# Optimization experiments

Hardware: AMD Instinct MI355X
Metric: run time of the kernel (lower is better)

Reference implementation:

```python
import jax, jax.numpy as jnp
import numpy as np

E, H, M = 1024, 16, 256
B, S = 2, 2048
D = E // H
SCALE = D ** -0.5


def setup_inputs() -> dict:
    key = jax.random.key(0)
    ks = jax.random.split(key, 10)
    p = 0.02
    return {
        "x": jax.random.normal(ks[0], (B, S, E), jnp.float32),
        "Wq": jax.random.normal(ks[1], (E, E), jnp.float32) * p,
        "bq": jax.random.normal(ks[2], (E,), jnp.float32) * p,
        "Wk": jax.random.normal(ks[3], (E, E), jnp.float32) * p,
        "bk": jax.random.normal(ks[4], (E,), jnp.float32) * p,
        "Wv": jax.random.normal(ks[5], (E, E), jnp.float32) * p,
        "bv": jax.random.normal(ks[6], (E,), jnp.float32) * p,
        "Wo": jax.random.normal(ks[7], (E, E), jnp.float32) * p,
        "bo": jax.random.normal(ks[8], (E,), jnp.float32) * p,
        "memory_state": jax.random.normal(ks[9], (M, E), jnp.float32) * p,
    }


def reference(x, Wq, bq, Wk, bk, Wv, bv, Wo, bo, memory_state):
    b, s, e = x.shape
    # QKV projections (torch Linear: y = x W^T + b), split heads -> [b,h,s,d]
    q = (x @ Wq.T + bq).reshape(b, s, H, D).transpose(0, 2, 1, 3)
    k = (x @ Wk.T + bk).reshape(b, s, H, D).transpose(0, 2, 1, 3)
    v = (x @ Wv.T + bv).reshape(b, s, H, D).transpose(0, 2, 1, 3)
    # full self-attention (eval mode: dropout is identity)
    attn = jax.nn.softmax(jnp.einsum("bhqd,bhkd->bhqk", q, k) * SCALE, axis=-1)
    attn_out = jnp.einsum("bhqk,bhkd->bhqd", attn, v)
    attn_out = attn_out.transpose(0, 2, 1, 3).reshape(b, s, e)
    # memory-read cross-attention on raw x against compressed memory [M,E]
    mem_w = jax.nn.softmax(jnp.einsum("bse,me->bsm", x, memory_state) * SCALE, axis=-1)
    mem_out = jnp.einsum("bsm,me->bse", mem_w, memory_state)
    out = attn_out + 0.5 * mem_out
    return out @ Wo.T + bo
```

## Files before the change

kernel.cpp:

```cpp
#include <hip/hip_runtime.h>
#include <cstdint>
#include <cstddef>


typedef __bf16 bf16;
typedef bf16  bf16x8 __attribute__((ext_vector_type(8)));
typedef bf16  bf16x4 __attribute__((ext_vector_type(4)));
typedef float f32x4  __attribute__((ext_vector_type(4)));
typedef int   i32x4  __attribute__((ext_vector_type(4)));

#define B_DIM 2
#define S_DIM 2048
#define E_DIM 1024
#define H_DIM 16
#define D_DIM 64
#define M_DIM 256
#define NROW  (B_DIM * S_DIM)
#define C1 0.18033688011112042f

__device__ __forceinline__ void async_cp16(const bf16* g, bf16* l)
{
    __builtin_amdgcn_global_load_lds(
        (const __attribute__((address_space(1))) void*)g,
        (__attribute__((address_space(3))) void*)l, 16, 0, 0);
}

__global__ void __launch_bounds__(256)
conv_all(const float* __restrict__ x,  const float* __restrict__ Wq,
         const float* __restrict__ Wk, const float* __restrict__ Wv,
         const float* __restrict__ Wo, const float* __restrict__ mem,
         bf16* __restrict__ xb,  bf16* __restrict__ Wqb,
         bf16* __restrict__ Wkb, bf16* __restrict__ Wvb,
         bf16* __restrict__ Wob, bf16* __restrict__ memb,
         bf16* __restrict__ memt)
{
    int t = blockIdx.x * 256 + threadIdx.x;
    const float* src; bf16* dst; int off; bool is_mem = false;
    if      (t <  524288) { src = x;   dst = xb;   off = t; }
    else if (t <  655360) { src = Wq;  dst = Wqb;  off = t - 524288; }
    else if (t <  786432) { src = Wk;  dst = Wkb;  off = t - 655360; }
    else if (t <  917504) { src = Wv;  dst = Wvb;  off = t - 786432; }
    else if (t < 1048576) { src = Wo;  dst = Wob;  off = t - 917504; }
    else                  { src = mem; dst = memb; off = t - 1048576; is_mem = true; }
    const float4* p = (const float4*)src + (size_t)off * 2;
    float4 a = p[0], b = p[1];
    bf16x8 o;
    o[0] = (bf16)a.x; o[1] = (bf16)a.y; o[2] = (bf16)a.z; o[3] = (bf16)a.w;
    o[4] = (bf16)b.x; o[5] = (bf16)b.y; o[6] = (bf16)b.z; o[7] = (bf16)b.w;
    *(bf16x8*)(dst + (size_t)off * 8) = o;
    if (is_mem) {
        int r = off >> 7, c0 = (off & 127) * 8;
        float h[8] = {a.x, a.y, a.z, a.w, b.x, b.y, b.z, b.w};
#pragma unroll
        for (int j = 0; j < 8; ++j)
            memt[(size_t)(c0 + j) * M_DIM + r] = (bf16)(0.5f * h[j]);
    }
}

struct GemmAcc { f32x4 a[4][4]; };

__device__ __forceinline__ void
gemm_core(const bf16* __restrict__ A, const bf16* __restrict__ Bm,
          int K, int m0, int n0, bf16* As, bf16* Bs, GemmAcc& R)
{
    const int tid  = threadIdx.x;
    const int lane = tid & 63;
    const int wave = tid >> 6;
    const int quad = lane >> 4;
    const int l16  = lane & 15;
    const int wm   = (wave >> 1) * 64;
    const int wn   = (wave & 1) * 64;

#pragma unroll
    for (int i = 0; i < 4; ++i)
#pragma unroll
        for (int j = 0; j < 4; ++j)
            R.a[i][j] = f32x4{0.f, 0.f, 0.f, 0.f};

    int s_c0  = wave * 128 + lane;
    int s_r0  = s_c0 >> 2;
    int s_k0  = (s_c0 & 3) ^ ((s_r0 >> 1) & 3);
    int s_c1  = s_c0 + 64;
    int s_r1  = s_c1 >> 2;
    int s_k1  = (s_c1 & 3) ^ ((s_r1 >> 1) & 3);
    const bf16* gA0 = A  + (size_t)(m0 + s_r0) * K + s_k0 * 8;
    const bf16* gA1 = A  + (size_t)(m0 + s_r1) * K + s_k1 * 8;
    const bf16* gB0 = Bm + (size_t)(n0 + s_r0) * K + s_k0 * 8;
    const bf16* gB1 = Bm + (size_t)(n0 + s_r1) * K + s_k1 * 8;

#define STAGE(buf, k0)                                                     \
    do {                                                                   \
        async_cp16(gA0 + (k0), &As[(buf) * 4096 + wave * 1024]);           \
        async_cp16(gA1 + (k0), &As[(buf) * 4096 + wave * 1024 + 512]);     \
        async_cp16(gB0 + (k0), &Bs[(buf) * 4096 + wave * 1024]);           \
        async_cp16(gB1 + (k0), &Bs[(buf) * 4096 + wave * 1024 + 512]);     \
    } while (0)

    STAGE(0, 0);
    int buf = 0;
    for (int k0 = 0; k0 < K; k0 += 32) {
        __syncthreads();
        if (k0 + 32 < K) STAGE(buf ^ 1, k0 + 32);

        const bf16* Ab = As + buf * 4096;
        const bf16* Bb = Bs + buf * 4096;
        bf16x8 af[4], bfr[4];
#pragma unroll
        for (int mi = 0; mi < 4; ++mi) {
            int m    = wm + mi * 16 + l16;
            int slot = quad ^ ((m >> 1) & 3);
            af[mi]   = *(const bf16x8*)(&Ab[(m * 4 + slot) * 8]);
        }
#pragma unroll
        for (int ni = 0; ni < 4; ++ni) {
            int n    = wn + ni * 16 + l16;
            int slot = quad ^ ((n >> 1) & 3);
            bfr[ni]  = *(const bf16x8*)(&Bb[(n * 4 + slot) * 8]);
        }
#pragma unroll
        for (int mi = 0; mi < 4; ++mi)
#pragma unroll
            for (int ni = 0; ni < 4; ++ni)
                R.a[mi][ni] = __builtin_amdgcn_mfma_f32_16x16x32_bf16(
                    af[mi], bfr[ni], R.a[mi][ni], 0, 0, 0);
        buf ^= 1;
    }
#undef STAGE
}

__global__ void __launch_bounds__(256, 3)
gemm_qkvl(const bf16* __restrict__ A,
          const bf16* __restrict__ Wq, const bf16* __restrict__ Wk,
          const bf16* __restrict__ Wv, const bf16* __restrict__ memb,
          const float* __restrict__ bq, const float* __restrict__ bk,
          const float* __restrict__ bv,
          bf16* __restrict__ q, bf16* __restrict__ k,
          bf16* __restrict__ vt, bf16* __restrict__ lg)
{
    __shared__ __align__(16) bf16 As[2 * 4096];
    __shared__ __align__(16) bf16 Bs[2 * 4096];
    const int lid  = blockIdx.x;
    const int xcd  = lid & 7;
    const int idx  = lid >> 3;
    const int mloc = idx / 26;
    const int nn   = idx - mloc * 26;
    const int m0   = (mloc * 8 + xcd) * 128;
    const int widx = (nn < 24) ? (nn >> 3) : 3;
    const int n0   = (nn < 24) ? (nn & 7) * 128 : (nn - 24) * 128;
    const bf16*  Bm = (widx == 0) ? Wq : (widx == 1) ? Wk :
                      (widx == 2) ? Wv : memb;
    GemmAcc R;
    gemm_core(A, Bm, E_DIM, m0, n0, As, Bs, R);

    const int lane = threadIdx.x & 63, wave = threadIdx.x >> 6;
    const int quad = lane >> 4, l16 = lane & 15;
    const int wm = (wave >> 1) * 64, wn = (wave & 1) * 64;

    if (widx == 0 || widx == 1) {
        bf16* C = (widx == 0) ? q : k;
        const float* bi = (widx == 0) ? bq : bk;
        float scale = (widx == 0) ? C1 : 1.0f;
#pragma unroll
        for (int ni = 0; ni < 4; ++ni) {
            int col  = n0 + wn + ni * 16 + l16;
            float bb = bi[col];
#pragma unroll
            for (int mi = 0; mi < 4; ++mi)
#pragma unroll
                for (int r = 0; r < 4; ++r) {
                    int rowg = m0 + wm + mi * 16 + quad * 4 + r;
                    C[(size_t)rowg * E_DIM + col] =
                        (bf16)((R.a[mi][ni][r] + bb) * scale);
                }
        }
    } else if (widx == 2) {
#pragma unroll
        for (int ni = 0; ni < 4; ++ni) {
            int col = n0 + wn + ni * 16 + l16;
            float bb = bv[col];
#pragma unroll
            for (int mi = 0; mi < 4; ++mi) {
                int row0 = m0 + wm + mi * 16 + quad * 4;
                int bidx = row0 >> 11, s = row0 & 2047;
                bf16x4 pk;
#pragma unroll
                for (int r = 0; r < 4; ++r) pk[r] = (bf16)(R.a[mi][ni][r] + bb);
                *(bf16x4*)(&vt[((size_t)(bidx * H_DIM) * 64 + col) * S_DIM + s]) = pk;
            }
        }
    } else {
#pragma unroll
        for (int ni = 0; ni < 4; ++ni) {
            int col = n0 + wn + ni * 16 + l16;
#pragma unroll
            for (int mi = 0; mi < 4; ++mi)
#pragma unroll
                for (int r = 0; r < 4; ++r) {
                    int rowg = m0 + wm + mi * 16 + quad * 4 + r;
                    lg[(size_t)rowg * M_DIM + col] = (bf16)R.a[mi][ni][r];
                }
        }
    }
}

__global__ void __launch_bounds__(256, 2)
gemm_out64(const bf16* __restrict__ A, const bf16* __restrict__ Bm,
           const float* __restrict__ bias, float* __restrict__ C)
{
    __shared__ __align__(16) bf16 As[2 * 2048];
    __shared__ __align__(16) bf16 Bs[2 * 4096];
    const int tid  = threadIdx.x;
    const int lane = tid & 63;
    const int wave = tid >> 6;
    const int quad = lane >> 4;
    const int l16  = lane & 15;
    const int wm   = (wave >> 1) * 32;
    const int wn   = (wave & 1) * 64;
    const int lid  = blockIdx.x;
    const int xcd  = lid & 7;
    const int idx  = lid >> 3;
    const int mloc = idx >> 3;
    const int nn   = idx & 7;
    const int m0   = (mloc * 8 + xcd) * 64;
    const int n0   = nn * 128;
    const int K    = E_DIM;

    f32x4 acc[2][4];
#pragma unroll
    for (int i = 0; i < 2; ++i)
#pragma unroll
        for (int j = 0; j < 4; ++j) acc[i][j] = f32x4{0.f, 0.f, 0.f, 0.f};

    int a_s  = wave * 64 + lane;
    int a_r  = a_s >> 2;
    int a_k  = (a_s & 3) ^ ((a_r >> 1) & 3);
    int b_s0 = wave * 128 + lane;
    int b_r0 = b_s0 >> 2;
    int b_k0 = (b_s0 & 3) ^ ((b_r0 >> 1) & 3);
    int b_s1 = b_s0 + 64;
    int b_r1 = b_s1 >> 2;
    int b_k1 = (b_s1 & 3) ^ ((b_r1 >> 1) & 3);
    const bf16* gA  = A  + (size_t)(m0 + a_r) * K + a_k * 8;
    const bf16* gB0 = Bm + (size_t)(n0 + b_r0) * K + b_k0 * 8;
    const bf16* gB1 = Bm + (size_t)(n0 + b_r1) * K + b_k1 * 8;

#define STAGE64(buf, k0)                                                   \
    do {                                                                   \
        async_cp16(gA  + (k0), &As[(buf) * 2048 + wave * 512]);            \
        async_cp16(gB0 + (k0), &Bs[(buf) * 4096 + wave * 1024]);           \
        async_cp16(gB1 + (k0), &Bs[(buf) * 4096 + wave * 1024 + 512]);     \
    } while (0)

    STAGE64(0, 0);
    int buf = 0;
    for (int k0 = 0; k0 < K; k0 += 32) {
        __syncthreads();
        if (k0 + 32 < K) STAGE64(buf ^ 1, k0 + 32);
        const bf16* Ab = As + buf * 2048;
        const bf16* Bb = Bs + buf * 4096;
        bf16x8 af[2], bfr[4];
#pragma unroll
        for (int mi = 0; mi < 2; ++mi) {
            int m    = wm + mi * 16 + l16;
            int slot = quad ^ ((m >> 1) & 3);
            af[mi]   = *(const bf16x8*)(&Ab[(m * 4 + slot) * 8]);
        }
#pragma unroll
        for (int ni = 0; ni < 4; ++ni) {
            int n    = wn + ni * 16 + l16;
            int slot = quad ^ ((n >> 1) & 3);
            bfr[ni]  = *(const bf16x8*)(&Bb[(n * 4 + slot) * 8]);
        }
#pragma unroll
        for (int mi = 0; mi < 2; ++mi)
#pragma unroll
            for (int ni = 0; ni < 4; ++ni)
                acc[mi][ni] = __builtin_amdgcn_mfma_f32_16x16x32_bf16(
                    af[mi], bfr[ni], acc[mi][ni], 0, 0, 0);
        buf ^= 1;
    }
#undef STAGE64

#pragma unroll
    for (int ni = 0; ni < 4; ++ni) {
        int col  = n0 + wn + ni * 16 + l16;
        float bb = bias[col];
#pragma unroll
        for (int mi = 0; mi < 2; ++mi)
#pragma unroll
            for (int r = 0; r < 4; ++r) {
                int rowg = m0 + wm + mi * 16 + quad * 4 + r;
                C[(size_t)rowg * E_DIM + col] = acc[mi][ni][r] + bb;
            }
    }
}

__global__ void __launch_bounds__(256, 4)
flash_attn(const bf16* __restrict__ q, const bf16* __restrict__ k,
           const bf16* __restrict__ vt, const bf16* __restrict__ lg,
           const bf16* __restrict__ memt, bf16* __restrict__ outc)
{
    __shared__ __align__(16) bf16 Ks[2 * 4096];
    __shared__ __align__(16) bf16 Vs[2 * 4096];
    __shared__ __align__(16) bf16 Ps[4 * 1024];
    const int tid  = threadIdx.x;
    const int lane = tid & 63;
    const int wave = tid >> 6;
    const int quad = lane >> 4;
    const int l16  = lane & 15;
    const int lid = blockIdx.x;
    const int xcd = lid & 7;
    const int kk  = lid >> 3;
    const int qt  = kk & 31;
    const int p   = ((kk >> 5) << 3) | xcd;
    const int b   = p >> 4;
    const int h   = p & 15;
    const int q0  = qt * 64 + wave * 16;

    const bf16* qb = q  + (size_t)(b * S_DIM + q0) * E_DIM + h * D_DIM;
    const bf16* kb = k  + (size_t)(b * S_DIM) * E_DIM + h * D_DIM;
    const bf16* vb = vt + (size_t)(b * H_DIM + h) * D_DIM * S_DIM;

    const int s_s0 = wave * 128 + lane;
    const int s_r0 = s_s0 >> 3;
    const int s_g0 = (s_s0 & 7) ^ (s_r0 & 7);
    const int s_s1 = s_s0 + 64;
    const int s_r1 = s_s1 >> 3;
    const int s_g1 = (s_s1 & 7) ^ (s_r1 & 7);
    const bf16* gK0 = kb + (size_t)s_r0 * E_DIM + s_g0 * 8;
    const bf16* gK1 = kb + (size_t)s_r1 * E_DIM + s_g1 * 8;
    const bf16* gV0 = vb + (size_t)s_r0 * S_DIM + s_g0 * 8;
    const bf16* gV1 = vb + (size_t)s_r1 * S_DIM + s_g1 * 8;

    bf16x8 a_q[2];
#pragma unroll
    for (int kc = 0; kc < 2; ++kc)
        a_q[kc] = *(const bf16x8*)(qb + (size_t)l16 * E_DIM + kc * 32 + quad * 8);

    bf16x8 vones;
#pragma unroll
    for (int j = 0; j < 8; ++j) vones[j] = (bf16)1.0f;

    f32x4 o_acc[4], osum;
#pragma unroll
    for (int i = 0; i < 4; ++i) o_acc[i] = f32x4{0.f, 0.f, 0.f, 0.f};
    osum = f32x4{0.f, 0.f, 0.f, 0.f};

    bf16* pw = Ps + wave * 1024;

    {
        i32x4 rK0 = *(const i32x4*)(gK0);
        i32x4 rK1 = *(const i32x4*)(gK1);
        i32x4 rV0 = *(const i32x4*)(gV0);
        i32x4 rV1 = *(const i32x4*)(gV1);
        bf16* dK = &Ks[wave * 1024 + lane * 8];
        bf16* dV = &Vs[wave * 1024 + lane * 8];
        *(i32x4*)dK         = rK0;
        *(i32x4*)(dK + 512) = rK1;
        *(i32x4*)dV         = rV0;
        *(i32x4*)(dV + 512) = rV1;
    }
    __syncthreads();

    int buf = 0;
    for (int kt = 0; kt < S_DIM; kt += 64) {
        const bool pre = (kt + 64 < S_DIM);
        i32x4 nK0, nK1, nV0, nV1;
        if (pre) {
            const size_t ko = (size_t)(kt + 64) * E_DIM;
            nK0 = *(const i32x4*)(gK0 + ko);
            nK1 = *(const i32x4*)(gK1 + ko);
            nV0 = *(const i32x4*)(gV0 + (kt + 64));
            nV1 = *(const i32x4*)(gV1 + (kt + 64));
        }
        const bf16* Kb = Ks + buf * 4096;
        const bf16* Vb = Vs + buf * 4096;

        f32x4 sc[4];
        __builtin_amdgcn_s_setprio(1);
#pragma unroll
        for (int nb = 0; nb < 4; ++nb) {
            int row = nb * 16 + l16;
            int sl0 = quad ^ (row & 7);
            int sl1 = (4 + quad) ^ (row & 7);
            bf16x8 bk0 = *(const bf16x8*)(&Kb[row * 64 + sl0 * 8]);
            bf16x8 bk1 = *(const bf16x8*)(&Kb[row * 64 + sl1 * 8]);
            f32x4 a = f32x4{0.f, 0.f, 0.f, 0.f};
            a = __builtin_amdgcn_mfma_f32_16x16x32_bf16(bk0, a_q[0], a, 0, 0, 0);
            a = __builtin_amdgcn_mfma_f32_16x16x32_bf16(bk1, a_q[1], a, 0, 0, 0);
            sc[nb] = a;
        }
        __builtin_amdgcn_s_setprio(0);

        bf16x8 bv[4][2];
#pragma unroll
        for (int nd = 0; nd < 4; ++nd)
#pragma unroll
            for (int kc = 0; kc < 2; ++kc) {
                int row  = nd * 16 + l16;
                int slot = (kc * 4 + quad) ^ (row & 7);
                bv[nd][kc] = *(const bf16x8*)(&Vb[row * 64 + slot * 8]);
            }

#pragma unroll
        for (int nb = 0; nb < 4; ++nb) {
            bf16x4 pk;
#pragma unroll
            for (int r = 0; r < 4; ++r) pk[r] = (bf16)exp2f(sc[nb][r]);
            int slot = (nb * 2 + (quad >> 1)) ^ (l16 & 7);
            *(bf16x4*)(&pw[l16 * 64 + slot * 8 + (quad & 1) * 4]) = pk;
        }

        bf16x8 a_p[2];
#pragma unroll
        for (int kc = 0; kc < 2; ++kc) {
            int slot = (kc * 4 + quad) ^ (l16 & 7);
            a_p[kc]  = *(const bf16x8*)(&pw[l16 * 64 + slot * 8]);
        }

        __builtin_amdgcn_s_setprio(1);
#pragma unroll
        for (int nd = 0; nd < 4; ++nd) {
            o_acc[nd] = __builtin_amdgcn_mfma_f32_16x16x32_bf16(
                a_p[0], bv[nd][0], o_acc[nd], 0, 0, 0);
            o_acc[nd] = __builtin_amdgcn_mfma_f32_16x16x32_bf16(
                a_p[1], bv[nd][1], o_acc[nd], 0, 0, 0);
        }
        osum = __builtin_amdgcn_mfma_f32_16x16x32_bf16(a_p[0], vones, osum, 0, 0, 0);
        osum = __builtin_amdgcn_mfma_f32_16x16x32_bf16(a_p[1], vones, osum, 0, 0, 0);
        __builtin_amdgcn_s_setprio(0);

        if (pre) {
            bf16* dK = &Ks[(buf ^ 1) * 4096 + wave * 1024 + lane * 8];
            bf16* dV = &Vs[(buf ^ 1) * 4096 + wave * 1024 + lane * 8];
            *(i32x4*)dK         = nK0;
            *(i32x4*)(dK + 512) = nK1;
            *(i32x4*)dV         = nV0;
            *(i32x4*)(dV + 512) = nV1;
        }
        __syncthreads();
        buf ^= 1;
    }

    float linv[4];
#pragma unroll
    for (int r = 0; r < 4; ++r) linv[r] = 1.f / osum[r];

    const bf16* Pr = lg   + (size_t)(b * S_DIM + q0) * M_DIM;
    const bf16* Mt = memt + (size_t)(h * D_DIM) * M_DIM;
    f32x4 macc[4], msum;
#pragma unroll
    for (int i = 0; i < 4; ++i) macc[i] = f32x4{0.f, 0.f, 0.f, 0.f};
    msum = f32x4{0.f, 0.f, 0.f, 0.f};
#pragma unroll
    for (int kc = 0; kc < 8; ++kc) {
        bf16x8 raw = *(const bf16x8*)(Pr + (size_t)l16 * M_DIM + kc * 32 + quad * 8);
        bf16x8 ep;
#pragma unroll
        for (int j = 0; j < 8; ++j) ep[j] = (bf16)exp2f(C1 * (float)raw[j]);
#pragma unroll
        for (int nd = 0; nd < 4; ++nd) {
            bf16x8 bm = *(const bf16x8*)(
                Mt + (size_t)(nd * 16 + l16) * M_DIM + kc * 32 + quad * 8);
            macc[nd] = __builtin_amdgcn_mfma_f32_16x16x32_bf16(
                ep, bm, macc[nd], 0, 0, 0);
        }
        msum = __builtin_amdgcn_mfma_f32_16x16x32_bf16(ep, vones, msum, 0, 0, 0);
    }

    bf16* ob = outc + (size_t)(b * S_DIM + q0) * E_DIM + h * D_DIM;
#pragma unroll
    for (int nd = 0; nd < 4; ++nd)
#pragma unroll
        for (int r = 0; r < 4; ++r) {
            size_t off = (size_t)(quad * 4 + r) * E_DIM + nd * 16 + l16;
            ob[off] = (bf16)(o_acc[nd][r] * linv[r] + macc[nd][r] / msum[r]);
        }
}

extern "C" void kernel_launch(void* const* d_in, const int* in_sizes, int n_in,
                              void* d_out, int out_size, void* d_ws, size_t ws_size,
                              hipStream_t stream)
{
    (void)in_sizes; (void)n_in; (void)out_size; (void)ws_size;
    const float* x   = (const float*)d_in[0];
    const float* Wq  = (const float*)d_in[1];
    const float* bq  = (const float*)d_in[2];
    const float* Wk  = (const float*)d_in[3];
    const float* bk  = (const float*)d_in[4];
    const float* Wv  = (const float*)d_in[5];
    const float* bv  = (const float*)d_in[6];
    const float* Wo  = (const float*)d_in[7];
    const float* bo  = (const float*)d_in[8];
    const float* mem = (const float*)d_in[9];
    float* out = (float*)d_out;

    bf16* w = (bf16*)d_ws;
    const size_t NE = (size_t)NROW * E_DIM;
    const size_t EE = (size_t)E_DIM * E_DIM;
    bf16* xb      = w;
    bf16* q_ws    = w + NE;
    bf16* k_ws    = w + 2 * NE;
    bf16* Wqb     = w + 3 * NE;
    bf16* Wkb     = Wqb + EE;
    bf16* Wvb     = Wkb + EE;
    bf16* Wob     = Wvb + EE;
    bf16* memb    = Wob + EE;
    bf16* lg_ws   = memb + (size_t)M_DIM * E_DIM;
    bf16* memt_ws = lg_ws + (size_t)NROW * M_DIM;
    bf16* vt_ws = (bf16*)d_out;

    dim3 blk(256);

    conv_all<<<dim3(4224), blk, 0, stream>>>(
        x, Wq, Wk, Wv, Wo, mem, xb, Wqb, Wkb, Wvb, Wob, memb, memt_ws);

    gemm_qkvl<<<dim3(832), blk, 0, stream>>>(
        xb, Wqb, Wkb, Wvb, memb, bq, bk, bv, q_ws, k_ws, vt_ws, lg_ws);

    flash_attn<<<dim3(1024), blk, 0, stream>>>(
        q_ws, k_ws, vt_ws, lg_ws, memt_ws, q_ws);

    gemm_out64<<<dim3(512), blk, 0, stream>>>(
        q_ws, Wob, bo, out);
}
```

Before: 222.9 us.

## Process two 16-row query groups per wave in flash attention

Each wave now handles 32 query rows (two groups of 16) instead of 16, so each block covers 128 queries and the grid halves to 512 blocks. K and V tiles loaded into LDS are reused across twice as many queries, halving global K/V traffic and LDS fill work per query. The cost is more registers per thread (launch bounds lowered to 2 blocks per SIMD set), fewer blocks to spread across CUs, and serialized P staging through the shared per-wave LDS buffer.

Measured after the change: 223.9 us. About the same (+0.5%).

```diff
diff --git a/kernel.cpp b/kernel.cpp
--- a/kernel.cpp
+++ b/kernel.cpp
@@ -295,7 +295,7 @@
     }
 }
 
-__global__ void __launch_bounds__(256, 4)
+__global__ void __launch_bounds__(256, 2)
 flash_attn(const bf16* __restrict__ q, const bf16* __restrict__ k,
            const bf16* __restrict__ vt, const bf16* __restrict__ lg,
            const bf16* __restrict__ memt, bf16* __restrict__ outc)
@@ -311,11 +311,11 @@
     const int lid = blockIdx.x;
     const int xcd = lid & 7;
     const int kk  = lid >> 3;
-    const int qt  = kk & 31;
-    const int p   = ((kk >> 5) << 3) | xcd;
+    const int qt  = kk & 15;
+    const int p   = ((kk >> 4) << 3) | xcd;
     const int b   = p >> 4;
     const int h   = p & 15;
-    const int q0  = qt * 64 + wave * 16;
+    const int q0  = qt * 128 + wave * 32;
 
     const bf16* qb = q  + (size_t)(b * S_DIM + q0) * E_DIM + h * D_DIM;
     const bf16* kb = k  + (size_t)(b * S_DIM) * E_DIM + h * D_DIM;
@@ -332,19 +332,25 @@
     const bf16* gV0 = vb + (size_t)s_r0 * S_DIM + s_g0 * 8;
     const bf16* gV1 = vb + (size_t)s_r1 * S_DIM + s_g1 * 8;
 
-    bf16x8 a_q[2];
-#pragma unroll
-    for (int kc = 0; kc < 2; ++kc)
-        a_q[kc] = *(const bf16x8*)(qb + (size_t)l16 * E_DIM + kc * 32 + quad * 8);
+    bf16x8 a_q[2][2];
+#pragma unroll
+    for (int g = 0; g < 2; ++g)
+#pragma unroll
+        for (int kc = 0; kc < 2; ++kc)
+            a_q[g][kc] = *(const bf16x8*)(
+                qb + (size_t)(g * 16 + l16) * E_DIM + kc * 32 + quad * 8);
 
     bf16x8 vones;
 #pragma unroll
     for (int j = 0; j < 8; ++j) vones[j] = (bf16)1.0f;
 
-    f32x4 o_acc[4], osum;
-#pragma unroll
-    for (int i = 0; i < 4; ++i) o_acc[i] = f32x4{0.f, 0.f, 0.f, 0.f};
-    osum = f32x4{0.f, 0.f, 0.f, 0.f};
+    f32x4 o_acc[2][4], osum[2];
+#pragma unroll
+    for (int g = 0; g < 2; ++g) {
+#pragma unroll
+        for (int i = 0; i < 4; ++i) o_acc[g][i] = f32x4{0.f, 0.f, 0.f, 0.f};
+        osum[g] = f32x4{0.f, 0.f, 0.f, 0.f};
+    }
 
     bf16* pw = Ps + wave * 1024;
 
@@ -376,7 +382,7 @@
         const bf16* Kb = Ks + buf * 4096;
         const bf16* Vb = Vs + buf * 4096;
 
-        f32x4 sc[4];
+        f32x4 sc[2][4];
         __builtin_amdgcn_s_setprio(1);
 #pragma unroll
         for (int nb = 0; nb < 4; ++nb) {
@@ -385,10 +391,13 @@
             int sl1 = (4 + quad) ^ (row & 7);
             bf16x8 bk0 = *(const bf16x8*)(&Kb[row * 64 + sl0 * 8]);
             bf16x8 bk1 = *(const bf16x8*)(&Kb[row * 64 + sl1 * 8]);
-            f32x4 a = f32x4{0.f, 0.f, 0.f, 0.f};
-            a = __builtin_amdgcn_mfma_f32_16x16x32_bf16(bk0, a_q[0], a, 0, 0, 0);
-            a = __builtin_amdgcn_mfma_f32_16x16x32_bf16(bk1, a_q[1], a, 0, 0, 0);
-            sc[nb] = a;
+#pragma unroll
+            for (int g = 0; g < 2; ++g) {
+                f32x4 a = f32x4{0.f, 0.f, 0.f, 0.f};
+                a = __builtin_amdgcn_mfma_f32_16x16x32_bf16(bk0, a_q[g][0], a, 0, 0, 0);
+                a = __builtin_amdgcn_mfma_f32_16x16x32_bf16(bk1, a_q[g][1], a, 0, 0, 0);
+                sc[g][nb] = a;
+            }
         }
         __builtin_amdgcn_s_setprio(0);
 
@@ -403,32 +412,33 @@
             }
 
 #pragma unroll
-        for (int nb = 0; nb < 4; ++nb) {
-            bf16x4 pk;
-#pragma unroll
-            for (int r = 0; r < 4; ++r) pk[r] = (bf16)exp2f(sc[nb][r]);
-            int slot = (nb * 2 + (quad >> 1)) ^ (l16 & 7);
-            *(bf16x4*)(&pw[l16 * 64 + slot * 8 + (quad & 1) * 4]) = pk;
-        }
-
-        bf16x8 a_p[2];
-#pragma unroll
-        for (int kc = 0; kc < 2; ++kc) {
-            int slot = (kc * 4 + quad) ^ (l16 & 7);
-            a_p[kc]  = *(const bf16x8*)(&pw[l16 * 64 + slot * 8]);
-        }
-
-        __builtin_amdgcn_s_setprio(1);
-#pragma unroll
-        for (int nd = 0; nd < 4; ++nd) {
-            o_acc[nd] = __builtin_amdgcn_mfma_f32_16x16x32_bf16(
-                a_p[0], bv[nd][0], o_acc[nd], 0, 0, 0);
-            o_acc[nd] = __builtin_amdgcn_mfma_f32_16x16x32_bf16(
-                a_p[1], bv[nd][1], o_acc[nd], 0, 0, 0);
-        }
-        osum = __builtin_amdgcn_mfma_f32_16x16x32_bf16(a_p[0], vones, osum, 0, 0, 0);
-        osum = __builtin_amdgcn_mfma_f32_16x16x32_bf16(a_p[1], vones, osum, 0, 0, 0);
-        __builtin_amdgcn_s_setprio(0);
+        for (int g = 0; g < 2; ++g) {
+#pragma unroll
+            for (int nb = 0; nb < 4; ++nb) {
+                bf16x4 pk;
+#pragma unroll
+                for (int r = 0; r < 4; ++r) pk[r] = (bf16)exp2f(sc[g][nb][r]);
+                int slot = (nb * 2 + (quad >> 1)) ^ (l16 & 7);
+                *(bf16x4*)(&pw[l16 * 64 + slot * 8 + (quad & 1) * 4]) = pk;
+            }
+            bf16x8 a_p[2];
+#pragma unroll
+            for (int kc = 0; kc < 2; ++kc) {
+                int slot = (kc * 4 + quad) ^ (l16 & 7);
+                a_p[kc]  = *(const bf16x8*)(&pw[l16 * 64 + slot * 8]);
+            }
+            __builtin_amdgcn_s_setprio(1);
+#pragma unroll
+            for (int nd = 0; nd < 4; ++nd) {
+                o_acc[g][nd] = __builtin_amdgcn_mfma_f32_16x16x32_bf16(
+                    a_p[0], bv[nd][0], o_acc[g][nd], 0, 0, 0);
+                o_acc[g][nd] = __builtin_amdgcn_mfma_f32_16x16x32_bf16(
+                    a_p[1], bv[nd][1], o_acc[g][nd], 0, 0, 0);
+            }
+            osum[g] = __builtin_amdgcn_mfma_f32_16x16x32_bf16(a_p[0], vones, osum[g], 0, 0, 0);
+            osum[g] = __builtin_amdgcn_mfma_f32_16x16x32_bf16(a_p[1], vones, osum[g], 0, 0, 0);
+            __builtin_amdgcn_s_setprio(0);
+        }
 
         if (pre) {
             bf16* dK = &Ks[(buf ^ 1) * 4096 + wave * 1024 + lane * 8];
@@ -442,40 +452,57 @@
         buf ^= 1;
     }
 
-    float linv[4];
-#pragma unroll
-    for (int r = 0; r < 4; ++r) linv[r] = 1.f / osum[r];
+    float linv[2][4];
+#pragma unroll
+    for (int g = 0; g < 2; ++g)
+#pragma unroll
+        for (int r = 0; r < 4; ++r) linv[g][r] = 1.f / osum[g][r];
 
     const bf16* Pr = lg   + (size_t)(b * S_DIM + q0) * M_DIM;
     const bf16* Mt = memt + (size_t)(h * D_DIM) * M_DIM;
-    f32x4 macc[4], msum;
-#pragma unroll
-    for (int i = 0; i < 4; ++i) macc[i] = f32x4{0.f, 0.f, 0.f, 0.f};
-    msum = f32x4{0.f, 0.f, 0.f, 0.f};
+    f32x4 macc[2][4], msum[2];
+#pragma unroll
+    for (int g = 0; g < 2; ++g) {
+#pragma unroll
+        for (int i = 0; i < 4; ++i) macc[g][i] = f32x4{0.f, 0.f, 0.f, 0.f};
+        msum[g] = f32x4{0.f, 0.f, 0.f, 0.f};
+    }
 #pragma unroll
     for (int kc = 0; kc < 8; ++kc) {
-        bf16x8 raw = *(const bf16x8*)(Pr + (size_t)l16 * M_DIM + kc * 32 + quad * 8);
-        bf16x8 ep;
-#pragma unroll
-        for (int j = 0; j < 8; ++j) ep[j] = (bf16)exp2f(C1 * (float)raw[j]);
+        bf16x8 ep[2];
+#pragma unroll
+        for (int g = 0; g < 2; ++g) {
+            bf16x8 raw = *(const bf16x8*)(
+                Pr + (size_t)(g * 16 + l16) * M_DIM + kc * 32 + quad * 8);
+#pragma unroll
+            for (int j = 0; j < 8; ++j) ep[g][j] = (bf16)exp2f(C1 * (float)raw[j]);
+        }
 #pragma unroll
         for (int nd = 0; nd < 4; ++nd) {
             bf16x8 bm = *(const bf16x8*)(
                 Mt + (size_t)(nd * 16 + l16) * M_DIM + kc * 32 + quad * 8);
-            macc[nd] = __builtin_amdgcn_mfma_f32_16x16x32_bf16(
-                ep, bm, macc[nd], 0, 0, 0);
-        }
-        msum = __builtin_amdgcn_mfma_f32_16x16x32_bf16(ep, vones, msum, 0, 0, 0);
+#pragma unroll
+            for (int g = 0; g < 2; ++g)
+                macc[g][nd] = __builtin_amdgcn_mfma_f32_16x16x32_bf16(
+                    ep[g], bm, macc[g][nd], 0, 0, 0);
+        }
+#pragma unroll
+        for (int g = 0; g < 2; ++g)
+            msum[g] = __builtin_amdgcn_mfma_f32_16x16x32_bf16(
+                ep[g], vones, msum[g], 0, 0, 0);
     }
 
     bf16* ob = outc + (size_t)(b * S_DIM + q0) * E_DIM + h * D_DIM;
 #pragma unroll
-    for (int nd = 0; nd < 4; ++nd)
-#pragma unroll
-        for (int r = 0; r < 4; ++r) {
-            size_t off = (size_t)(quad * 4 + r) * E_DIM + nd * 16 + l16;
-            ob[off] = (bf16)(o_acc[nd][r] * linv[r] + macc[nd][r] / msum[r]);
-        }
+    for (int g = 0; g < 2; ++g)
+#pragma unroll
+        for (int nd = 0; nd < 4; ++nd)
+#pragma unroll
+            for (int r = 0; r < 4; ++r) {
+                size_t off = (size_t)(g * 16 + quad * 4 + r) * E_DIM + nd * 16 + l16;
+                ob[off] = (bf16)(o_acc[g][nd][r] * linv[g][r]
+                                 + macc[g][nd][r] / msum[g][r]);
+            }
 }
 
 extern "C" void kernel_launch(void* const* d_in, const int* in_sizes, int n_in,
@@ -518,7 +545,7 @@
     gemm_qkvl<<<dim3(832), blk, 0, stream>>>(
         xb, Wqb, Wkb, Wvb, memb, bq, bk, bv, q_ws, k_ws, vt_ws, lg_ws);
 
-    flash_attn<<<dim3(1024), blk, 0, stream>>>(
+    flash_attn<<<dim3(512), blk, 0, stream>>>(
         q_ws, k_ws, vt_ws, lg_ws, memt_ws, q_ws);
 
     gemm_out64<<<dim3(512), blk, 0, stream>>>(
```

## Rewrite flash attention with 32x32x16 MFMA and register-resident P operand

Applied to the files above, without the earlier changes.

Switches the attention kernel from 16x16x32 to 32x32x16 bf16 MFMA, with each wave handling 32 query rows and blocks covering 128 queries, so the grid is halved. The score accumulator layout is arranged so exp'd probabilities feed the PV MFMA directly from registers, removing the LDS round-trip through the P scratch buffer. V tiles are stored into LDS with a new split 8-byte swizzled layout to match the new operand layout. The change raises register pressure (launch bounds lowered to 2 blocks per SM) and reduces occupancy and the number of blocks in flight.

Result: faster. 215.1 us (-3.5%).

```diff
diff --git a/kernel.cpp b/kernel.cpp
--- a/kernel.cpp
+++ b/kernel.cpp
@@ -7,7 +7,9 @@
 typedef bf16  bf16x8 __attribute__((ext_vector_type(8)));
 typedef bf16  bf16x4 __attribute__((ext_vector_type(4)));
 typedef float f32x4  __attribute__((ext_vector_type(4)));
+typedef float f32x16 __attribute__((ext_vector_type(16)));
 typedef int   i32x4  __attribute__((ext_vector_type(4)));
+typedef int   i32x2  __attribute__((ext_vector_type(2)));
 
 #define B_DIM 2
 #define S_DIM 2048
@@ -17,6 +19,16 @@
 #define M_DIM 256
 #define NROW  (B_DIM * S_DIM)
 #define C1 0.18033688011112042f
+
+#define MFMA32(a, b, c) __builtin_amdgcn_mfma_f32_32x32x16_bf16((a), (b), (c), 0, 0, 0)
+
+__device__ __forceinline__ f32x16 zero16()
+{
+    f32x16 z;
+#pragma unroll
+    for (int i = 0; i < 16; ++i) z[i] = 0.f;
+    return z;
+}
 
 __device__ __forceinline__ void async_cp16(const bf16* g, bf16* l)
 {
@@ -295,27 +307,26 @@
     }
 }
 
-__global__ void __launch_bounds__(256, 4)
+__global__ void __launch_bounds__(256, 2)
 flash_attn(const bf16* __restrict__ q, const bf16* __restrict__ k,
            const bf16* __restrict__ vt, const bf16* __restrict__ lg,
            const bf16* __restrict__ memt, bf16* __restrict__ outc)
 {
     __shared__ __align__(16) bf16 Ks[2 * 4096];
     __shared__ __align__(16) bf16 Vs[2 * 4096];
-    __shared__ __align__(16) bf16 Ps[4 * 1024];
     const int tid  = threadIdx.x;
     const int lane = tid & 63;
     const int wave = tid >> 6;
-    const int quad = lane >> 4;
-    const int l16  = lane & 15;
+    const int hi   = lane >> 5;
+    const int l32  = lane & 31;
     const int lid = blockIdx.x;
     const int xcd = lid & 7;
     const int kk  = lid >> 3;
-    const int qt  = kk & 31;
-    const int p   = ((kk >> 5) << 3) | xcd;
+    const int qt  = kk & 15;
+    const int p   = ((kk >> 4) << 3) | xcd;
     const int b   = p >> 4;
     const int h   = p & 15;
-    const int q0  = qt * 64 + wave * 16;
+    const int q0  = qt * 128 + wave * 32;
 
     const bf16* qb = q  + (size_t)(b * S_DIM + q0) * E_DIM + h * D_DIM;
     const bf16* kb = k  + (size_t)(b * S_DIM) * E_DIM + h * D_DIM;
@@ -332,33 +343,34 @@
     const bf16* gV0 = vb + (size_t)s_r0 * S_DIM + s_g0 * 8;
     const bf16* gV1 = vb + (size_t)s_r1 * S_DIM + s_g1 * 8;
 
-    bf16x8 a_q[2];
-#pragma unroll
-    for (int kc = 0; kc < 2; ++kc)
-        a_q[kc] = *(const bf16x8*)(qb + (size_t)l16 * E_DIM + kc * 32 + quad * 8);
+    const int kd0 = wave * 1024 + lane * 8;
+    const int v00 = s_r0 * 64 + (((s_g0 & ~1)    ) ^ (s_r0 & 7)) * 8 + (s_g0 & 1) * 4;
+    const int v01 = s_r0 * 64 + (((s_g0 & ~1) | 1) ^ (s_r0 & 7)) * 8 + (s_g0 & 1) * 4;
+    const int v10 = s_r1 * 64 + (((s_g1 & ~1)    ) ^ (s_r1 & 7)) * 8 + (s_g1 & 1) * 4;
+    const int v11 = s_r1 * 64 + (((s_g1 & ~1) | 1) ^ (s_r1 & 7)) * 8 + (s_g1 & 1) * 4;
+
+    bf16x8 qfr[4];
+#pragma unroll
+    for (int c = 0; c < 4; ++c)
+        qfr[c] = *(const bf16x8*)(qb + (size_t)l32 * E_DIM + c * 16 + hi * 8);
 
     bf16x8 vones;
 #pragma unroll
     for (int j = 0; j < 8; ++j) vones[j] = (bf16)1.0f;
 
-    f32x4 o_acc[4], osum;
-#pragma unroll
-    for (int i = 0; i < 4; ++i) o_acc[i] = f32x4{0.f, 0.f, 0.f, 0.f};
-    osum = f32x4{0.f, 0.f, 0.f, 0.f};
-
-    bf16* pw = Ps + wave * 1024;
+    f32x16 o_acc0 = zero16(), o_acc1 = zero16(), osum = zero16();
 
     {
         i32x4 rK0 = *(const i32x4*)(gK0);
         i32x4 rK1 = *(const i32x4*)(gK1);
         i32x4 rV0 = *(const i32x4*)(gV0);
         i32x4 rV1 = *(const i32x4*)(gV1);
-        bf16* dK = &Ks[wave * 1024 + lane * 8];
-        bf16* dV = &Vs[wave * 1024 + lane * 8];
-        *(i32x4*)dK         = rK0;
-        *(i32x4*)(dK + 512) = rK1;
-        *(i32x4*)dV         = rV0;
-        *(i32x4*)(dV + 512) = rV1;
+        *(i32x4*)(&Ks[kd0])       = rK0;
+        *(i32x4*)(&Ks[kd0 + 512]) = rK1;
+        *(i32x2*)(&Vs[v00]) = i32x2{rV0[0], rV0[1]};
+        *(i32x2*)(&Vs[v01]) = i32x2{rV0[2], rV0[3]};
+        *(i32x2*)(&Vs[v10]) = i32x2{rV1[0], rV1[1]};
+        *(i32x2*)(&Vs[v11]) = i32x2{rV1[2], rV1[3]};
     }
     __syncthreads();
 
@@ -376,106 +388,82 @@
         const bf16* Kb = Ks + buf * 4096;
         const bf16* Vb = Vs + buf * 4096;
 
-        f32x4 sc[4];
+        f32x16 sc0 = zero16(), sc1 = zero16();
         __builtin_amdgcn_s_setprio(1);
 #pragma unroll
-        for (int nb = 0; nb < 4; ++nb) {
-            int row = nb * 16 + l16;
-            int sl0 = quad ^ (row & 7);
-            int sl1 = (4 + quad) ^ (row & 7);
-            bf16x8 bk0 = *(const bf16x8*)(&Kb[row * 64 + sl0 * 8]);
-            bf16x8 bk1 = *(const bf16x8*)(&Kb[row * 64 + sl1 * 8]);
-            f32x4 a = f32x4{0.f, 0.f, 0.f, 0.f};
-            a = __builtin_amdgcn_mfma_f32_16x16x32_bf16(bk0, a_q[0], a, 0, 0, 0);
-            a = __builtin_amdgcn_mfma_f32_16x16x32_bf16(bk1, a_q[1], a, 0, 0, 0);
-            sc[nb] = a;
+        for (int c = 0; c < 4; ++c) {
+            const int cc  = c * 2 + hi;
+            const int swz = (cc ^ (l32 & 7)) * 8;
+            bf16x8 kf0 = *(const bf16x8*)(&Kb[l32 * 64 + swz]);
+            bf16x8 kf1 = *(const bf16x8*)(&Kb[(32 + l32) * 64 + swz]);
+            sc0 = MFMA32(kf0, qfr[c], sc0);
+            sc1 = MFMA32(kf1, qfr[c], sc1);
         }
         __builtin_amdgcn_s_setprio(0);
 
-        bf16x8 bv[4][2];
-#pragma unroll
-        for (int nd = 0; nd < 4; ++nd)
-#pragma unroll
-            for (int kc = 0; kc < 2; ++kc) {
-                int row  = nd * 16 + l16;
-                int slot = (kc * 4 + quad) ^ (row & 7);
-                bv[nd][kc] = *(const bf16x8*)(&Vb[row * 64 + slot * 8]);
-            }
-
-#pragma unroll
-        for (int nb = 0; nb < 4; ++nb) {
-            bf16x4 pk;
-#pragma unroll
-            for (int r = 0; r < 4; ++r) pk[r] = (bf16)exp2f(sc[nb][r]);
-            int slot = (nb * 2 + (quad >> 1)) ^ (l16 & 7);
-            *(bf16x4*)(&pw[l16 * 64 + slot * 8 + (quad & 1) * 4]) = pk;
-        }
-
-        bf16x8 a_p[2];
-#pragma unroll
-        for (int kc = 0; kc < 2; ++kc) {
-            int slot = (kc * 4 + quad) ^ (l16 & 7);
-            a_p[kc]  = *(const bf16x8*)(&pw[l16 * 64 + slot * 8]);
+        bf16x8 ap[4];
+#pragma unroll
+        for (int kc = 0; kc < 4; ++kc) {
+            const f32x16 sct = (kc < 2) ? sc0 : sc1;
+            const int base = (kc & 1) * 8;
+#pragma unroll
+            for (int j = 0; j < 8; ++j)
+                ap[kc][j] = (bf16)exp2f(sct[base + j]);
         }
 
         __builtin_amdgcn_s_setprio(1);
 #pragma unroll
-        for (int nd = 0; nd < 4; ++nd) {
-            o_acc[nd] = __builtin_amdgcn_mfma_f32_16x16x32_bf16(
-                a_p[0], bv[nd][0], o_acc[nd], 0, 0, 0);
-            o_acc[nd] = __builtin_amdgcn_mfma_f32_16x16x32_bf16(
-                a_p[1], bv[nd][1], o_acc[nd], 0, 0, 0);
-        }
-        osum = __builtin_amdgcn_mfma_f32_16x16x32_bf16(a_p[0], vones, osum, 0, 0, 0);
-        osum = __builtin_amdgcn_mfma_f32_16x16x32_bf16(a_p[1], vones, osum, 0, 0, 0);
+        for (int kc = 0; kc < 4; ++kc) {
+            const int swz = ((kc * 2 + hi) ^ (l32 & 7)) * 8;
+            bf16x8 vf0 = *(const bf16x8*)(&Vb[l32 * 64 + swz]);
+            bf16x8 vf1 = *(const bf16x8*)(&Vb[(32 + l32) * 64 + swz]);
+            o_acc0 = MFMA32(ap[kc], vf0, o_acc0);
+            o_acc1 = MFMA32(ap[kc], vf1, o_acc1);
+            osum   = MFMA32(ap[kc], vones, osum);
+        }
         __builtin_amdgcn_s_setprio(0);
 
         if (pre) {
-            bf16* dK = &Ks[(buf ^ 1) * 4096 + wave * 1024 + lane * 8];
-            bf16* dV = &Vs[(buf ^ 1) * 4096 + wave * 1024 + lane * 8];
-            *(i32x4*)dK         = nK0;
-            *(i32x4*)(dK + 512) = nK1;
-            *(i32x4*)dV         = nV0;
-            *(i32x4*)(dV + 512) = nV1;
+            const int bo = (buf ^ 1) * 4096;
+            *(i32x4*)(&Ks[bo + kd0])       = nK0;
+            *(i32x4*)(&Ks[bo + kd0 + 512]) = nK1;
+            *(i32x2*)(&Vs[bo + v00]) = i32x2{nV0[0], nV0[1]};
+            *(i32x2*)(&Vs[bo + v01]) = i32x2{nV0[2], nV0[3]};
+            *(i32x2*)(&Vs[bo + v10]) = i32x2{nV1[0], nV1[1]};
+            *(i32x2*)(&Vs[bo + v11]) = i32x2{nV1[2], nV1[3]};
         }
         __syncthreads();
         buf ^= 1;
     }
 
-    float linv[4];
-#pragma unroll
-    for (int r = 0; r < 4; ++r) linv[r] = 1.f / osum[r];
+    float linv[16];
+#pragma unroll
+    for (int r = 0; r < 16; ++r) linv[r] = 1.f / osum[r];
 
     const bf16* Pr = lg   + (size_t)(b * S_DIM + q0) * M_DIM;
     const bf16* Mt = memt + (size_t)(h * D_DIM) * M_DIM;
-    f32x4 macc[4], msum;
-#pragma unroll
-    for (int i = 0; i < 4; ++i) macc[i] = f32x4{0.f, 0.f, 0.f, 0.f};
-    msum = f32x4{0.f, 0.f, 0.f, 0.f};
-#pragma unroll
-    for (int kc = 0; kc < 8; ++kc) {
-        bf16x8 raw = *(const bf16x8*)(Pr + (size_t)l16 * M_DIM + kc * 32 + quad * 8);
-        bf16x8 ep;
-#pragma unroll
-        for (int j = 0; j < 8; ++j) ep[j] = (bf16)exp2f(C1 * (float)raw[j]);
-#pragma unroll
-        for (int nd = 0; nd < 4; ++nd) {
-            bf16x8 bm = *(const bf16x8*)(
-                Mt + (size_t)(nd * 16 + l16) * M_DIM + kc * 32 + quad * 8);
-            macc[nd] = __builtin_amdgcn_mfma_f32_16x16x32_bf16(
-                ep, bm, macc[nd], 0, 0, 0);
-        }
-        msum = __builtin_amdgcn_mfma_f32_16x16x32_bf16(ep, vones, msum, 0, 0, 0);
+    f32x16 macc0 = zero16(), macc1 = zero16(), msum = zero16();
+#pragma unroll
+    for (int mc = 0; mc < 16; ++mc) {
+        bf16x8 raw = *(const bf16x8*)(Pr + (size_t)l32 * M_DIM + mc * 16 + hi * 8);
+        bf16x8 epv;
+#pragma unroll
+        for (int j = 0; j < 8; ++j) epv[j] = (bf16)exp2f(C1 * (float)raw[j]);
+        bf16x8 bm0 = *(const bf16x8*)(Mt + (size_t)l32 * M_DIM        + mc * 16 + hi * 8);
+        bf16x8 bm1 = *(const bf16x8*)(Mt + (size_t)(32 + l32) * M_DIM + mc * 16 + hi * 8);
+        macc0 = MFMA32(epv, bm0, macc0);
+        macc1 = MFMA32(epv, bm1, macc1);
+        msum  = MFMA32(epv, vones, msum);
     }
 
     bf16* ob = outc + (size_t)(b * S_DIM + q0) * E_DIM + h * D_DIM;
 #pragma unroll
-    for (int nd = 0; nd < 4; ++nd)
-#pragma unroll
-        for (int r = 0; r < 4; ++r) {
-            size_t off = (size_t)(quad * 4 + r) * E_DIM + nd * 16 + l16;
-            ob[off] = (bf16)(o_acc[nd][r] * linv[r] + macc[nd][r] / msum[r]);
-        }
+    for (int r = 0; r < 16; ++r) {
+        const int qrow = (r & 3) + 8 * (r >> 2) + 4 * hi;
+        const float mi = 1.f / msum[r];
+        ob[(size_t)qrow * E_DIM + l32]      = (bf16)(o_acc0[r] * linv[r] + macc0[r] * mi);
+        ob[(size_t)qrow * E_DIM + 32 + l32] = (bf16)(o_acc1[r] * linv[r] + macc1[r] * mi);
+    }
 }
 
 extern "C" void kernel_launch(void* const* d_in, const int* in_sizes, int n_in,
@@ -518,7 +506,7 @@
     gemm_qkvl<<<dim3(832), blk, 0, stream>>>(
         xb, Wqb, Wkb, Wvb, memb, bq, bk, bv, q_ws, k_ws, vt_ws, lg_ws);
 
-    flash_attn<<<dim3(1024), blk, 0, stream>>>(
+    flash_attn<<<dim3(512), blk, 0, stream>>>(
         q_ws, k_ws, vt_ws, lg_ws, memt_ws, q_ws);
 
     gemm_out64<<<dim3(512), blk, 0, stream>>>(
```
